# Kernel tuning notes

Hardware: AMD Instinct MI355X
Metric: run time of the kernel (lower is better)

## Reference

```python
import jax, jax.numpy as jnp
import numpy as np

H = 2048          # hidden size
N_HEADS = 16
HEAD_DIM = H // N_HEADS   # 128
ATTN_SCALE = 8.0          # attention_scale > 1.0 -> custom max-subtract path
B, S = 2, 2048


def setup_inputs() -> dict:
    key = jax.random.key(0)
    k1, k2, k3, k4, k5 = jax.random.split(key, 5)
    hidden_states = jax.random.normal(k1, (B, S, H), dtype=jnp.float32)
    # causal left-to-right multiplicative mask, broadcast over batch and heads
    ltor_mask = jnp.tril(jnp.ones((S, S), dtype=jnp.float32))[None, None]
    std = 0.02
    W_qkv = jax.random.normal(k2, (H, 3 * H), dtype=jnp.float32) * std
    b_qkv = jnp.zeros((3 * H,), dtype=jnp.float32)
    W_out = jax.random.normal(k3, (H, H), dtype=jnp.float32) * std
    b_out = jnp.zeros((H,), dtype=jnp.float32)
    return {"hidden_states": hidden_states, "ltor_mask": ltor_mask,
            "W_qkv": W_qkv, "b_qkv": b_qkv, "W_out": W_out, "b_out": b_out}


def reference(hidden_states, ltor_mask, W_qkv, b_qkv, W_out, b_out):
    b, s, h = hidden_states.shape
    # fused QKV projection: [b, s, 3h]
    qkv = jnp.einsum('bsh,hk->bsk', hidden_states, W_qkv) + b_qkv
    q, k, v = jnp.split(qkv, 3, axis=-1)
    # [b, s, h] -> [b, n, s, hn]
    def to_heads(t):
        return t.reshape(b, s, N_HEADS, HEAD_DIM).transpose(0, 2, 1, 3)
    q, k, v = to_heads(q), to_heads(k), to_heads(v)
    # custom scale: q / sqrt(scale), k / sqrt(hn * scale)
    inv = 1.0 / (ATTN_SCALE * np.sqrt(np.float32(HEAD_DIM)))
    scores = jnp.einsum('bnqd,bnkd->bnqk', q, k) * jnp.float32(inv)
    # multiplicative mask BEFORE max-subtract (zeroes masked positions)
    scores = scores * ltor_mask
    # attention_scale > 1.0 path: subtract row max, re-multiply by scale
    scores = (scores - jnp.max(scores, axis=-1, keepdims=True)) * jnp.float32(ATTN_SCALE)
    # additive large-negative fill on masked entries
    scores = scores + jnp.float32(-65504.0) * (1.0 - ltor_mask)
    probs = jax.nn.softmax(scores, axis=-1)
    ctx = jnp.einsum('bnqk,bnkd->bnqd', probs, v)
    ctx = ctx.transpose(0, 2, 1, 3).reshape(b, s, h)
    out = jnp.einsum('bsh,hk->bsk', ctx, W_out) + b_out
    return out
```

## Files before the change

### kernel.cpp

```cpp
#include <hip/hip_runtime.h>

#define S_LEN 2048
#define HDIM  2048
#define NHEADS 16
#define DHEAD 128
#define BATCH 2
#define MROWS (BATCH * S_LEN)
#define QKVN  (3 * HDIM)

typedef _Float16 f16;
typedef _Float16 f16x8 __attribute__((ext_vector_type(8)));
typedef _Float16 f16x4 __attribute__((ext_vector_type(4)));
typedef float    f32x4 __attribute__((ext_vector_type(4)));
typedef float    f32x16 __attribute__((ext_vector_type(16)));

typedef const __attribute__((address_space(1))) void* gas_ptr;
typedef __attribute__((address_space(3))) void*       las_ptr;

#define MFMA16(a, b, c)  __builtin_amdgcn_mfma_f32_16x16x32_f16(a, b, c, 0, 0, 0)
#define MFMA32(a, b, c)  __builtin_amdgcn_mfma_f32_32x32x16_f16(a, b, c, 0, 0, 0)

__device__ __forceinline__ void gl_lds16(const f16* g, f16* lds_wave_base) {
#if defined(__has_builtin) && __has_builtin(__builtin_amdgcn_global_load_lds)
  __builtin_amdgcn_global_load_lds((gas_ptr)g, (las_ptr)lds_wave_base, 16, 0, 0);
#else
  int lane = threadIdx.x & 63;
  ((f16x8*)lds_wave_base)[lane] = *(const f16x8*)g;
#endif
}


__global__ __launch_bounds__(256) void cvt_blocked_kernel(const float* __restrict__ X,
                                                          f16* __restrict__ Xb) {
  int kt = blockIdx.x;
  int rt = blockIdx.y;
  int t = threadIdx.x;
  int m = t >> 1, half = t & 1;
  const float* src = X + (size_t)(rt * 128 + m) * HDIM + kt * 32 + half * 16;
  float4 v0 = ((const float4*)src)[0];
  float4 v1 = ((const float4*)src)[1];
  float4 v2 = ((const float4*)src)[2];
  float4 v3 = ((const float4*)src)[3];
  f16x8 a = {(f16)v0.x, (f16)v0.y, (f16)v0.z, (f16)v0.w,
             (f16)v1.x, (f16)v1.y, (f16)v1.z, (f16)v1.w};
  f16x8 b = {(f16)v2.x, (f16)v2.y, (f16)v2.z, (f16)v2.w,
             (f16)v3.x, (f16)v3.y, (f16)v3.z, (f16)v3.w};
  f16* dst = Xb + ((size_t)rt * 64 + kt) * 4096 + ((half * 2) * 128 + m) * 8;
  *(f16x8*)dst = a;
  *(f16x8*)(dst + 1024) = b;
}

__global__ __launch_bounds__(256) void transpose_cvt_blocked_kernel(
    const float* __restrict__ W, f16* __restrict__ Wb, int K, int N) {
  __shared__ float tile[64][65];
  int k0 = blockIdx.y * 64, n0 = blockIdx.x * 64;
  int tr = threadIdx.x >> 4;
  int tc = (threadIdx.x & 15) * 4;
  int KT = K >> 5;
#pragma unroll
  for (int rr = 0; rr < 4; ++rr) {
    int r = rr * 16 + tr;
    float4 v = *(const float4*)(W + (size_t)(k0 + r) * N + n0 + tc);
    tile[r][tc + 0] = v.x; tile[r][tc + 1] = v.y;
    tile[r][tc + 2] = v.z; tile[r][tc + 3] = v.w;
  }
  __syncthreads();
#pragma unroll
  for (int rr = 0; rr < 4; ++rr) {
    int r = rr * 16 + tr;
    int n = n0 + r;
    int kBase = k0 + tc;
    f16x4 o;
#pragma unroll
    for (int c = 0; c < 4; ++c) o[c] = (f16)tile[tc + c][r];
    int nt = n >> 7, nn = n & 127;
    int kt = kBase >> 5, kc = (kBase >> 3) & 3, j = kBase & 7;
    *(f16x4*)(Wb + ((size_t)nt * KT + kt) * 4096 + (kc * 128 + nn) * 8 + j) = o;
  }
}

template <int MODE>
__global__ __launch_bounds__(256) void gemm_kernel(const f16* __restrict__ Ablk,
                                                   const f16* __restrict__ Bblk,
                                                   const float* __restrict__ bias,
                                                   float* __restrict__ Cout,
                                                   f16* __restrict__ Qr,
                                                   f16* __restrict__ KB,
                                                   f16* __restrict__ VB,
                                                   int M, int N, int K) {
  __shared__ f16 As[4 * 128 * 8];
  __shared__ f16 Bs[4 * 128 * 8];
  int tid = threadIdx.x;
  int lane = tid & 63, w = tid >> 6;
  int lhi = lane >> 4, llo = lane & 15;
  int m0 = blockIdx.y * 128, n0 = blockIdx.x * 128;
  int wm = (w & 1) * 64, wn = (w >> 1) * 64;
  int KT = K >> 5;
  const f16* Ab = Ablk + (size_t)blockIdx.y * KT * 4096;
  const f16* Bb = Bblk + (size_t)blockIdx.x * KT * 4096;

  f32x4 acc[4][4];
#pragma unroll
  for (int i = 0; i < 4; ++i)
#pragma unroll
    for (int j = 0; j < 4; ++j) acc[i][j] = (f32x4){0.f, 0.f, 0.f, 0.f};

  for (int kt = 0; kt < KT; ++kt) {
    __syncthreads();
#pragma unroll
    for (int i2 = 0; i2 < 2; ++i2) {
      int Lw = i2 * 256 + w * 64;
      gl_lds16(Ab + (size_t)kt * 4096 + Lw * 8 + (lane * 8), As + Lw * 8);
      gl_lds16(Bb + (size_t)kt * 4096 + Lw * 8 + (lane * 8), Bs + Lw * 8);
    }
    __syncthreads();

    f16x8 af[4], bf[4];
#pragma unroll
    for (int i = 0; i < 4; ++i)
      af[i] = *(const f16x8*)(As + (lhi * 128 + wm + i * 16 + llo) * 8);
#pragma unroll
    for (int j = 0; j < 4; ++j)
      bf[j] = *(const f16x8*)(Bs + (lhi * 128 + wn + j * 16 + llo) * 8);
#pragma unroll
    for (int i = 0; i < 4; ++i)
#pragma unroll
      for (int j = 0; j < 4; ++j) acc[i][j] = MFMA16(af[i], bf[j], acc[i][j]);
  }

#pragma unroll
  for (int j = 0; j < 4; ++j) {
    int col = n0 + wn + j * 16 + llo;
    float bv = bias[col];
#pragma unroll
    for (int i = 0; i < 4; ++i) {
      int rowb = m0 + wm + i * 16 + lhi * 4;
      if (MODE == 0) {
#pragma unroll
        for (int r = 0; r < 4; ++r)
          Cout[(size_t)(rowb + r) * N + col] = acc[i][j][r] + bv;
      } else {
        int region = n0 >> 11;
        if (region == 0) {
#pragma unroll
          for (int r = 0; r < 4; ++r)
            Qr[(size_t)(rowb + r) * HDIM + col] = (f16)(acc[i][j][r] + bv);
        } else if (region == 1) {
          int cK = col - HDIM;
          int hd = cK >> 7, d = cK & 127, g = d >> 3, dj = d & 7;
#pragma unroll
          for (int r = 0; r < 4; ++r) {
            int row = rowb + r;
            int b = row >> 11, s = row & 2047;
            int kt2 = s >> 6, key = s & 63;
            size_t addr = ((((size_t)(b * 16 + hd) * 32 + kt2) * 16 + g) * 64 + key) * 8 + dj;
            KB[addr] = (f16)(acc[i][j][r] + bv);
          }
        } else {
          int cV = col - 2 * HDIM;
          int hd = cV >> 7, d = cV & 127;
          int row = rowb;
          int b = row >> 11, s = row & 2047;
          int kt2 = s >> 6, key = s & 63;
          int kg = key >> 3, kj = key & 7;
          f16x4 pv = {(f16)(acc[i][j][0] + bv), (f16)(acc[i][j][1] + bv),
                      (f16)(acc[i][j][2] + bv), (f16)(acc[i][j][3] + bv)};
          size_t addr = ((((size_t)(b * 16 + hd) * 32 + kt2) * 8 + kg) * 128 + d) * 8 + kj;
          *(f16x4*)(VB + addr) = pv;
        }
      }
    }
  }
}

__global__ __launch_bounds__(256, 3) void attn_kernel(const f16* __restrict__ Qr,
                                                      const f16* __restrict__ KB,
                                                      const f16* __restrict__ VB,
                                                      f16* __restrict__ Opart,
                                                      float* __restrict__ Lpart) {
  __shared__ f16 Ks[1024 * 8];
  __shared__ f16 Vs[1024 * 8];
  __shared__ f16 Ps[4][32 * 72];

  int tid = threadIdx.x, lane = tid & 63, w = tid >> 6;
  int l5 = lane & 31, hl = lane >> 5;
  int bh = blockIdx.y, b = bh >> 4, hd = bh & 15;
  int gx = blockIdx.x;
  int qt, kt0, kt1, slot;
  if (gx < 8) { qt = gx; slot = 0; kt0 = 0; kt1 = 2 * qt + 2; }
  else {
    qt = 8 + ((gx - 8) >> 1); slot = (gx - 8) & 1;
    kt0 = slot ? (qt + 1) : 0;
    kt1 = slot ? (2 * qt + 2) : (qt + 1);
  }

  int qbase = qt * 128 + w * 32;
  int qrow = qbase + l5;

  const f16* qp = Qr + (size_t)(b * S_LEN + qrow) * HDIM + hd * DHEAD + hl * 8;
  f16x8 qf[8];
#pragma unroll
  for (int s8 = 0; s8 < 8; ++s8) qf[s8] = *(const f16x8*)(qp + s8 * 16);

  f32x16 oac[4];
#pragma unroll
  for (int mt = 0; mt < 4; ++mt)
#pragma unroll
    for (int r = 0; r < 16; ++r) oac[mt][r] = 0.f;
  float rs = 0.f;

  const float C1 = 0.12752747419986393f;
  const float C2 = 11.541560327111708f;

  const f16* KBb = KB + (size_t)bh * 32 * 8192;
  const f16* VBb = VB + (size_t)bh * 32 * 8192;

  for (int kt = kt0; kt < kt1; ++kt) {
    __syncthreads();
    {
      const f16* Kt = KBb + (size_t)kt * 8192;
      const f16* Vt = VBb + (size_t)kt * 8192;
#pragma unroll
      for (int c = 0; c < 4; ++c) {
        int u0 = w * 256 + c * 64;
        gl_lds16(Kt + (size_t)(u0 + lane) * 8, Ks + u0 * 8);
        gl_lds16(Vt + (size_t)(u0 + lane) * 8, Vs + u0 * 8);
      }
    }
    __syncthreads();

    if (kt * 64 <= qbase + 31) {
      f32x16 sac[2];
#pragma unroll
      for (int mt = 0; mt < 2; ++mt)
#pragma unroll
        for (int r = 0; r < 16; ++r) sac[mt][r] = 0.f;
#pragma unroll
      for (int s8 = 0; s8 < 8; ++s8) {
#pragma unroll
        for (int mt = 0; mt < 2; ++mt) {
          f16x8 kf = *(const f16x8*)(Ks + ((s8 * 2 + hl) * 64 + mt * 32 + l5) * 8);
          sac[mt] = MFMA32(kf, qf[s8], sac[mt]);
        }
      }

      bool diag = (kt * 64 + 63 > qbase);
#pragma unroll
      for (int mt = 0; mt < 2; ++mt) {
#pragma unroll
        for (int g4 = 0; g4 < 4; ++g4) {
          f16x4 pk;
#pragma unroll
          for (int r = 0; r < 4; ++r) {
            int keyl = mt * 32 + g4 * 8 + hl * 4 + r;
            float p = __builtin_amdgcn_exp2f(fmaf(sac[mt][g4 * 4 + r], C1, -C2));
            if (diag && (kt * 64 + keyl > qrow)) p = 0.f;
            rs += p;
            pk[r] = (f16)p;
          }
          *(f16x4*)(&Ps[w][l5 * 72 + mt * 32 + g4 * 8 + hl * 4]) = pk;
        }
      }
      asm volatile("s_waitcnt lgkmcnt(0)" ::: "memory");

#pragma unroll
      for (int ks = 0; ks < 4; ++ks) {
        f16x8 pf = *(const f16x8*)(&Ps[w][l5 * 72 + ks * 16 + hl * 8]);
#pragma unroll
        for (int mt = 0; mt < 4; ++mt) {
          f16x8 vf = *(const f16x8*)(Vs + ((ks * 2 + hl) * 128 + mt * 32 + l5) * 8);
          oac[mt] = MFMA32(vf, pf, oac[mt]);
        }
      }
    }
  }

  float lsum = rs + __shfl_xor(rs, 32, 64);
  size_t ob = ((size_t)slot * 32 + bh) * S_LEN * DHEAD + (size_t)qrow * DHEAD;
#pragma unroll
  for (int mt = 0; mt < 4; ++mt) {
#pragma unroll
    for (int g4 = 0; g4 < 4; ++g4) {
      int d = mt * 32 + g4 * 8 + hl * 4;
      f16x4 ov = {(f16)oac[mt][g4 * 4 + 0], (f16)oac[mt][g4 * 4 + 1],
                  (f16)oac[mt][g4 * 4 + 2], (f16)oac[mt][g4 * 4 + 3]};
      *(f16x4*)(Opart + ob + d) = ov;
    }
  }
  if (hl == 0) Lpart[((size_t)slot * 32 + bh) * S_LEN + qrow] = lsum;
}

__global__ __launch_bounds__(256) void merge_kernel(const f16* __restrict__ Opart,
                                                    const float* __restrict__ Lpart,
                                                    f16* __restrict__ CTXb) {
  int t = blockIdx.x * 256 + threadIdx.x;
  int d8 = (t & 15) * 8;
  int q = (t >> 4) & 2047;
  int bh = t >> 15;
  int b = bh >> 4, hd = bh & 15;
  int ns = ((q >> 7) >= 8) ? 2 : 1;
  size_t o0 = ((size_t)bh * S_LEN + q) * DHEAD + d8;
  const size_t OSLOT = (size_t)32 * S_LEN * DHEAD;
  float l = Lpart[(size_t)bh * S_LEN + q];
  f16x8 a = *(const f16x8*)(Opart + o0);
  float acc[8];
#pragma unroll
  for (int j = 0; j < 8; ++j) acc[j] = (float)a[j];
  if (ns == 2) {
    l += Lpart[OSLOT / DHEAD + (size_t)bh * S_LEN + q];
    f16x8 a2 = *(const f16x8*)(Opart + OSLOT + o0);
#pragma unroll
    for (int j = 0; j < 8; ++j) acc[j] += (float)a2[j];
  }
  float inv = 1.0f / l;
  f16x8 o;
#pragma unroll
  for (int j = 0; j < 8; ++j) o[j] = (f16)(acc[j] * inv);
  int row = b * S_LEN + q;
  int col = hd * DHEAD + d8;
  int rt = row >> 7, rr = row & 127;
  int kt = col >> 5, kc = (col >> 3) & 3;
  *(f16x8*)(CTXb + ((size_t)rt * 64 + kt) * 4096 + (kc * 128 + rr) * 8) = o;
}

extern "C" void kernel_launch(void* const* d_in, const int* in_sizes, int n_in,
                              void* d_out, int out_size, void* d_ws, size_t ws_size,
                              hipStream_t stream) {
  const float* X    = (const float*)d_in[0];
  const float* Wqkv = (const float*)d_in[2];
  const float* bqkv = (const float*)d_in[3];
  const float* Wout = (const float*)d_in[4];
  const float* bout = (const float*)d_in[5];
  float* out = (float*)d_out;

  char* ws = (char*)d_ws;
  f16* Xb    = (f16*)ws;  ws += (size_t)MROWS * HDIM * sizeof(f16);
  f16* Wqkvb = (f16*)ws;  ws += (size_t)QKVN * HDIM * sizeof(f16);
  f16* Woutb = (f16*)ws;  ws += (size_t)HDIM * HDIM * sizeof(f16);
  f16* Qr    = (f16*)ws;  ws += (size_t)MROWS * HDIM * sizeof(f16);
  f16* KB    = (f16*)ws;  ws += (size_t)32 * 32 * 8192 * sizeof(f16);
  f16* VB    = (f16*)ws;  ws += (size_t)32 * 32 * 8192 * sizeof(f16);
  f16* Opart = (f16*)ws;  ws += (size_t)2 * 32 * S_LEN * DHEAD * sizeof(f16);
  float* Lpart = (float*)ws;  ws += (size_t)2 * 32 * S_LEN * sizeof(float);
  f16* CTXb = Xb;

  cvt_blocked_kernel<<<dim3(HDIM / 32, MROWS / 128), 256, 0, stream>>>(X, Xb);
  transpose_cvt_blocked_kernel<<<dim3(QKVN / 64, HDIM / 64), 256, 0, stream>>>(Wqkv, Wqkvb, HDIM, QKVN);
  transpose_cvt_blocked_kernel<<<dim3(HDIM / 64, HDIM / 64), 256, 0, stream>>>(Wout, Woutb, HDIM, HDIM);

  gemm_kernel<1><<<dim3(QKVN / 128, MROWS / 128), 256, 0, stream>>>(
      Xb, Wqkvb, bqkv, nullptr, Qr, KB, VB, MROWS, QKVN, HDIM);

  attn_kernel<<<dim3(24, 32), 256, 0, stream>>>(Qr, KB, VB, Opart, Lpart);

  merge_kernel<<<(32 * S_LEN * 16) / 256, 256, 0, stream>>>(Opart, Lpart, CTXb);

  gemm_kernel<0><<<dim3(HDIM / 128, MROWS / 128), 256, 0, stream>>>(
      CTXb, Woutb, bout, out, nullptr, nullptr, nullptr, MROWS, HDIM, HDIM);
}
```

Baseline: 416.5 us.

## Split attention into single-wave 32-row blocks and split-K the output GEMM

The attention kernel changes from 4-wave 128-query blocks that stage K/V in LDS to single-wave 32-query blocks that read K/V straight from global memory. The causal key range is split into 1–4 segments by query position, which gives 160 blocks per head and a more even load. The output projection GEMM is split along K into two halves written as f16 partials, and a new merge kernel adds them together with the bias. This raises parallelism for the small 256-block output GEMM, at the cost of extra partial traffic, f16 rounding of the partials, and no LDS reuse of K/V across waves.

```diff
diff --git a/kernel.cpp b/kernel.cpp
--- a/kernel.cpp
+++ b/kernel.cpp
@@ -83,7 +83,7 @@
 __global__ __launch_bounds__(256) void gemm_kernel(const f16* __restrict__ Ablk,
                                                    const f16* __restrict__ Bblk,
                                                    const float* __restrict__ bias,
-                                                   float* __restrict__ Cout,
+                                                   f16* __restrict__ Cpart,
                                                    f16* __restrict__ Qr,
                                                    f16* __restrict__ KB,
                                                    f16* __restrict__ VB,
@@ -99,13 +99,16 @@
   const f16* Ab = Ablk + (size_t)blockIdx.y * KT * 4096;
   const f16* Bb = Bblk + (size_t)blockIdx.x * KT * 4096;
 
+  int ktBeg = 0, ktEnd = KT;
+  if (MODE == 2) { int half = KT >> 1; ktBeg = blockIdx.z * half; ktEnd = ktBeg + half; }
+
   f32x4 acc[4][4];
 #pragma unroll
   for (int i = 0; i < 4; ++i)
 #pragma unroll
     for (int j = 0; j < 4; ++j) acc[i][j] = (f32x4){0.f, 0.f, 0.f, 0.f};
 
-  for (int kt = 0; kt < KT; ++kt) {
+  for (int kt = ktBeg; kt < ktEnd; ++kt) {
     __syncthreads();
 #pragma unroll
     for (int i2 = 0; i2 < 2; ++i2) {
@@ -131,14 +134,15 @@
 #pragma unroll
   for (int j = 0; j < 4; ++j) {
     int col = n0 + wn + j * 16 + llo;
-    float bv = bias[col];
+    float bv = (MODE == 1) ? bias[col] : 0.f;
 #pragma unroll
     for (int i = 0; i < 4; ++i) {
       int rowb = m0 + wm + i * 16 + lhi * 4;
-      if (MODE == 0) {
+      if (MODE == 2) {
+        size_t zoff = (size_t)blockIdx.z * M * N;
 #pragma unroll
         for (int r = 0; r < 4; ++r)
-          Cout[(size_t)(rowb + r) * N + col] = acc[i][j][r] + bv;
+          Cpart[zoff + (size_t)(rowb + r) * N + col] = (f16)acc[i][j][r];
       } else {
         int region = n0 >> 11;
         if (region == 0) {
@@ -173,28 +177,48 @@
   }
 }
 
-__global__ __launch_bounds__(256, 3) void attn_kernel(const f16* __restrict__ Qr,
-                                                      const f16* __restrict__ KB,
-                                                      const f16* __restrict__ VB,
-                                                      f16* __restrict__ Opart,
-                                                      float* __restrict__ Lpart) {
-  __shared__ f16 Ks[1024 * 8];
-  __shared__ f16 Vs[1024 * 8];
-  __shared__ f16 Ps[4][32 * 72];
-
-  int tid = threadIdx.x, lane = tid & 63, w = tid >> 6;
+__global__ __launch_bounds__(256) void merge_out_kernel(const f16* __restrict__ Cpart,
+                                                        const float* __restrict__ bias,
+                                                        float* __restrict__ out) {
+  int t = blockIdx.x * 256 + threadIdx.x;
+  int col8 = (t & 255) * 8;
+  int row = t >> 8;
+  size_t base = (size_t)row * HDIM + col8;
+  const size_t MN = (size_t)MROWS * HDIM;
+  f16x8 a = *(const f16x8*)(Cpart + base);
+  f16x8 b = *(const f16x8*)(Cpart + MN + base);
+  float4 b0 = *(const float4*)(bias + col8);
+  float4 b1 = *(const float4*)(bias + col8 + 4);
+  float4 o0 = {(float)a[0] + (float)b[0] + b0.x, (float)a[1] + (float)b[1] + b0.y,
+               (float)a[2] + (float)b[2] + b0.z, (float)a[3] + (float)b[3] + b0.w};
+  float4 o1 = {(float)a[4] + (float)b[4] + b1.x, (float)a[5] + (float)b[5] + b1.y,
+               (float)a[6] + (float)b[6] + b1.z, (float)a[7] + (float)b[7] + b1.w};
+  *(float4*)(out + base) = o0;
+  *(float4*)(out + base + 4) = o1;
+}
+
+__global__ __launch_bounds__(64, 3) void attn_kernel(const f16* __restrict__ Qr,
+                                                     const f16* __restrict__ KB,
+                                                     const f16* __restrict__ VB,
+                                                     f16* __restrict__ Opart,
+                                                     float* __restrict__ Lpart) {
+  __shared__ f16 Ps[32 * 72];
+
+  int lane = threadIdx.x;
   int l5 = lane & 31, hl = lane >> 5;
   int bh = blockIdx.y, b = bh >> 4, hd = bh & 15;
   int gx = blockIdx.x;
-  int qt, kt0, kt1, slot;
-  if (gx < 8) { qt = gx; slot = 0; kt0 = 0; kt1 = 2 * qt + 2; }
-  else {
-    qt = 8 + ((gx - 8) >> 1); slot = (gx - 8) & 1;
-    kt0 = slot ? (qt + 1) : 0;
-    kt1 = slot ? (2 * qt + 2) : (qt + 1);
-  }
-
-  int qbase = qt * 128 + w * 32;
+
+  int qt2, seg, nseg;
+  if (gx < 16)      { qt2 = gx;                    seg = 0;            nseg = 1; }
+  else if (gx < 48) { qt2 = 16 + ((gx - 16) >> 1); seg = (gx - 16) & 1; nseg = 2; }
+  else if (gx < 96) { int r = gx - 48; qt2 = 32 + r / 3; seg = r % 3;   nseg = 3; }
+  else              { int r = gx - 96; qt2 = 48 + (r >> 2); seg = r & 3; nseg = 4; }
+  int cnt = (qt2 >> 1) + 1;
+  int kt0 = (seg * cnt) / nseg;
+  int kt1 = ((seg + 1) * cnt) / nseg;
+
+  int qbase = qt2 * 32;
   int qrow = qbase + l5;
 
   const f16* qp = Qr + (size_t)(b * S_LEN + qrow) * HDIM + hd * DHEAD + hl * 8;
@@ -216,67 +240,54 @@
   const f16* VBb = VB + (size_t)bh * 32 * 8192;
 
   for (int kt = kt0; kt < kt1; ++kt) {
-    __syncthreads();
-    {
-      const f16* Kt = KBb + (size_t)kt * 8192;
-      const f16* Vt = VBb + (size_t)kt * 8192;
-#pragma unroll
-      for (int c = 0; c < 4; ++c) {
-        int u0 = w * 256 + c * 64;
-        gl_lds16(Kt + (size_t)(u0 + lane) * 8, Ks + u0 * 8);
-        gl_lds16(Vt + (size_t)(u0 + lane) * 8, Vs + u0 * 8);
+    const f16* Kt = KBb + (size_t)kt * 8192;
+    const f16* Vt = VBb + (size_t)kt * 8192;
+
+    f32x16 sac0, sac1;
+#pragma unroll
+    for (int r = 0; r < 16; ++r) { sac0[r] = 0.f; sac1[r] = 0.f; }
+#pragma unroll
+    for (int s8 = 0; s8 < 8; ++s8) {
+      f16x8 kf0 = *(const f16x8*)(Kt + ((s8 * 2 + hl) * 64 + l5) * 8);
+      f16x8 kf1 = *(const f16x8*)(Kt + ((s8 * 2 + hl) * 64 + 32 + l5) * 8);
+      sac0 = MFMA32(kf0, qf[s8], sac0);
+      sac1 = MFMA32(kf1, qf[s8], sac1);
+    }
+
+    bool diag = (kt * 64 + 63 > qbase);
+#pragma unroll
+    for (int mt = 0; mt < 2; ++mt) {
+#pragma unroll
+      for (int g4 = 0; g4 < 4; ++g4) {
+        f16x4 pk;
+#pragma unroll
+        for (int r = 0; r < 4; ++r) {
+          float sv = (mt == 0) ? sac0[g4 * 4 + r] : sac1[g4 * 4 + r];
+          int keyl = mt * 32 + g4 * 8 + hl * 4 + r;
+          float p = __builtin_amdgcn_exp2f(fmaf(sv, C1, -C2));
+          if (diag && (kt * 64 + keyl > qrow)) p = 0.f;
+          rs += p;
+          pk[r] = (f16)p;
+        }
+        *(f16x4*)(&Ps[l5 * 72 + mt * 32 + g4 * 8 + hl * 4]) = pk;
       }
     }
-    __syncthreads();
-
-    if (kt * 64 <= qbase + 31) {
-      f32x16 sac[2];
-#pragma unroll
-      for (int mt = 0; mt < 2; ++mt)
-#pragma unroll
-        for (int r = 0; r < 16; ++r) sac[mt][r] = 0.f;
-#pragma unroll
-      for (int s8 = 0; s8 < 8; ++s8) {
-#pragma unroll
-        for (int mt = 0; mt < 2; ++mt) {
-          f16x8 kf = *(const f16x8*)(Ks + ((s8 * 2 + hl) * 64 + mt * 32 + l5) * 8);
-          sac[mt] = MFMA32(kf, qf[s8], sac[mt]);
-        }
+    asm volatile("s_waitcnt lgkmcnt(0)" ::: "memory");
+
+#pragma unroll
+    for (int ks = 0; ks < 4; ++ks) {
+      f16x8 pf = *(const f16x8*)(&Ps[l5 * 72 + ks * 16 + hl * 8]);
+#pragma unroll
+      for (int mt = 0; mt < 4; ++mt) {
+        f16x8 vf = *(const f16x8*)(Vt + ((ks * 2 + hl) * 128 + mt * 32 + l5) * 8);
+        oac[mt] = MFMA32(vf, pf, oac[mt]);
       }
-
-      bool diag = (kt * 64 + 63 > qbase);
-#pragma unroll
-      for (int mt = 0; mt < 2; ++mt) {
-#pragma unroll
-        for (int g4 = 0; g4 < 4; ++g4) {
-          f16x4 pk;
-#pragma unroll
-          for (int r = 0; r < 4; ++r) {
-            int keyl = mt * 32 + g4 * 8 + hl * 4 + r;
-            float p = __builtin_amdgcn_exp2f(fmaf(sac[mt][g4 * 4 + r], C1, -C2));
-            if (diag && (kt * 64 + keyl > qrow)) p = 0.f;
-            rs += p;
-            pk[r] = (f16)p;
-          }
-          *(f16x4*)(&Ps[w][l5 * 72 + mt * 32 + g4 * 8 + hl * 4]) = pk;
-        }
-      }
-      asm volatile("s_waitcnt lgkmcnt(0)" ::: "memory");
-
-#pragma unroll
-      for (int ks = 0; ks < 4; ++ks) {
-        f16x8 pf = *(const f16x8*)(&Ps[w][l5 * 72 + ks * 16 + hl * 8]);
-#pragma unroll
-        for (int mt = 0; mt < 4; ++mt) {
-          f16x8 vf = *(const f16x8*)(Vs + ((ks * 2 + hl) * 128 + mt * 32 + l5) * 8);
-          oac[mt] = MFMA32(vf, pf, oac[mt]);
-        }
-      }
     }
   }
 
   float lsum = rs + __shfl_xor(rs, 32, 64);
-  size_t ob = ((size_t)slot * 32 + bh) * S_LEN * DHEAD + (size_t)qrow * DHEAD;
+  size_t slot = (size_t)bh * 160 + gx;
+  size_t ob = slot * (32 * DHEAD) + (size_t)l5 * DHEAD;
 #pragma unroll
   for (int mt = 0; mt < 4; ++mt) {
 #pragma unroll
@@ -287,7 +298,7 @@
       *(f16x4*)(Opart + ob + d) = ov;
     }
   }
-  if (hl == 0) Lpart[((size_t)slot * 32 + bh) * S_LEN + qrow] = lsum;
+  if (hl == 0) Lpart[slot * 32 + l5] = lsum;
 }
 
 __global__ __launch_bounds__(256) void merge_kernel(const f16* __restrict__ Opart,
@@ -298,19 +309,23 @@
   int q = (t >> 4) & 2047;
   int bh = t >> 15;
   int b = bh >> 4, hd = bh & 15;
-  int ns = ((q >> 7) >= 8) ? 2 : 1;
-  size_t o0 = ((size_t)bh * S_LEN + q) * DHEAD + d8;
-  const size_t OSLOT = (size_t)32 * S_LEN * DHEAD;
-  float l = Lpart[(size_t)bh * S_LEN + q];
-  f16x8 a = *(const f16x8*)(Opart + o0);
+  int qt2 = q >> 5, l5 = q & 31;
+  int ns = (qt2 >> 4) + 1;
+  int gxbase;
+  if (qt2 < 16)      gxbase = qt2;
+  else if (qt2 < 32) gxbase = 2 * qt2 - 16;
+  else if (qt2 < 48) gxbase = 3 * qt2 - 48;
+  else               gxbase = 4 * qt2 - 96;
+  size_t slot0 = (size_t)bh * 160 + gxbase;
   float acc[8];
 #pragma unroll
-  for (int j = 0; j < 8; ++j) acc[j] = (float)a[j];
-  if (ns == 2) {
-    l += Lpart[OSLOT / DHEAD + (size_t)bh * S_LEN + q];
-    f16x8 a2 = *(const f16x8*)(Opart + OSLOT + o0);
-#pragma unroll
-    for (int j = 0; j < 8; ++j) acc[j] += (float)a2[j];
+  for (int j = 0; j < 8; ++j) acc[j] = 0.f;
+  float l = 0.f;
+  for (int s = 0; s < ns; ++s) {
+    l += Lpart[(slot0 + s) * 32 + l5];
+    f16x8 a = *(const f16x8*)(Opart + (slot0 + s) * (32 * DHEAD) + (size_t)l5 * DHEAD + d8);
+#pragma unroll
+    for (int j = 0; j < 8; ++j) acc[j] += (float)a[j];
   }
   float inv = 1.0f / l;
   f16x8 o;
@@ -340,9 +355,10 @@
   f16* Qr    = (f16*)ws;  ws += (size_t)MROWS * HDIM * sizeof(f16);
   f16* KB    = (f16*)ws;  ws += (size_t)32 * 32 * 8192 * sizeof(f16);
   f16* VB    = (f16*)ws;  ws += (size_t)32 * 32 * 8192 * sizeof(f16);
-  f16* Opart = (f16*)ws;  ws += (size_t)2 * 32 * S_LEN * DHEAD * sizeof(f16);
-  float* Lpart = (float*)ws;  ws += (size_t)2 * 32 * S_LEN * sizeof(float);
-  f16* CTXb = Xb;
+  f16* Opart = (f16*)ws;  ws += (size_t)32 * 160 * 32 * DHEAD * sizeof(f16);
+  float* Lpart = (float*)ws;  ws += (size_t)32 * 160 * 32 * sizeof(float);
+  f16* CTXb  = Xb;
+  f16* Cpart = Opart;
 
   cvt_blocked_kernel<<<dim3(HDIM / 32, MROWS / 128), 256, 0, stream>>>(X, Xb);
   transpose_cvt_blocked_kernel<<<dim3(QKVN / 64, HDIM / 64), 256, 0, stream>>>(Wqkv, Wqkvb, HDIM, QKVN);
@@ -351,10 +367,12 @@
   gemm_kernel<1><<<dim3(QKVN / 128, MROWS / 128), 256, 0, stream>>>(
       Xb, Wqkvb, bqkv, nullptr, Qr, KB, VB, MROWS, QKVN, HDIM);
 
-  attn_kernel<<<dim3(24, 32), 256, 0, stream>>>(Qr, KB, VB, Opart, Lpart);
+  attn_kernel<<<dim3(160, 32), 64, 0, stream>>>(Qr, KB, VB, Opart, Lpart);
 
   merge_kernel<<<(32 * S_LEN * 16) / 256, 256, 0, stream>>>(Opart, Lpart, CTXb);
 
-  gemm_kernel<0><<<dim3(HDIM / 128, MROWS / 128), 256, 0, stream>>>(
-      CTXb, Woutb, bout, out, nullptr, nullptr, nullptr, MROWS, HDIM, HDIM);
-}
+  gemm_kernel<2><<<dim3(HDIM / 128, MROWS / 128, 2), 256, 0, stream>>>(
+      CTXb, Woutb, nullptr, Cpart, nullptr, nullptr, nullptr, MROWS, HDIM, HDIM);
+
+  merge_out_kernel<<<(MROWS * HDIM / 8) / 256, 256, 0, stream>>>(Cpart, bout, out);
+}
```

Result: slower. 465.3 us (+11.7%).
